# Kernel tuning notes

Measured on AMD Instinct MI355X. Metric: run time of the kernel, lower is better.

The kernel has to match this reference:

```python
import jax, jax.numpy as jnp
import numpy as np
import math

B, CF, H, W = 2, 64, 256, 256
CH = 32          # 'channel' init arg
KS, DIL, PAD = 3, 2, 2
IMG_H, IMG_W = 512, 512


def _pos_encode(h, w, d_model):
    # Sinusoidal encoding along x and y, interleaved sin/cos -> [2*d_model, h, w]
    div = jnp.exp(jnp.arange(0, d_model, 2, dtype=jnp.float32) * (-math.log(10000.0) / d_model))  # [d/2]
    ax = jnp.arange(w, dtype=jnp.float32)[None, :] * div[:, None]   # [d/2, w]
    ay = jnp.arange(h, dtype=jnp.float32)[None, :] * div[:, None]   # [d/2, h]
    x = jnp.stack([jnp.sin(ax), jnp.cos(ax)], axis=1).reshape(d_model, w)  # even=sin, odd=cos
    y = jnp.stack([jnp.sin(ay), jnp.cos(ay)], axis=1).reshape(d_model, h)
    x = jnp.broadcast_to(x[:, None, :], (d_model, h, w))
    y = jnp.broadcast_to(y[:, :, None], (d_model, h, w))
    return jnp.concatenate([x, y], axis=0)  # [2*d_model, h, w]


def _unfold3x3(x):
    # F.unfold(kernel=3, dilation=2, padding=2, stride=1) -> [B, C, 9, H, W]
    b, c, h, w = x.shape
    xp = jnp.pad(x, ((0, 0), (0, 0), (PAD, PAD), (PAD, PAD)))
    offs = (0, DIL, 2 * DIL)
    patches = [xp[:, :, i:i + h, j:j + w] for i in offs for j in offs]  # row-major kernel order
    return jnp.stack(patches, axis=2)


def setup_inputs() -> dict:
    key = jax.random.key(0)
    k1, k2, k3, k4, k5 = jax.random.split(key, 5)
    return {
        "inp": jax.random.normal(k1, (B, CF, H, W), dtype=jnp.float32),
        "img": jax.random.uniform(k2, (B, 3, IMG_H, IMG_W), dtype=jnp.float32),
        "w_pos": jax.random.normal(k3, (CH, 2 * CH), dtype=jnp.float32) * 0.1,
        "w_img": jax.random.normal(k4, (CH, 3), dtype=jnp.float32) * 0.1,
        "w_comp": jax.random.normal(k5, (CF,), dtype=jnp.float32) * 0.1,
    }


def reference(inp, img, w_pos, w_img, w_comp):
    b, cf, h, w = inp.shape
    # positional embedding -> 1x1 conv (channel matmul)
    pos = _pos_encode(h, w, CH)                                   # [2*CH, H, W]
    pos_embd = jnp.einsum('oc,chw->ohw', w_pos, pos)              # [CH, H, W]
    pos_embd = jnp.broadcast_to(pos_embd[None], (b, CH, h, w))
    # bilinear resize of image to feature resolution, then 1x1 conv
    rimg = jax.image.resize(img, (b, 3, h, w), method='bilinear')
    rimg = jnp.einsum('oc,bchw->bohw', w_img, rimg)               # [B, CH, H, W]
    em = jnp.concatenate([rimg, pos_embd], axis=1)                # [B, 2*CH, H, W]
    # neighborhood similarity score
    un_em = _unfold3x3(em)                                        # [B, 2CH, 9, H, W]
    feature_score = jnp.einsum('bckhw,bchw->bkhw', un_em, em)     # [B, 9, H, W]
    # feature compatibility: 1x1 conv (dot with w_comp) per neighbor, sigmoid
    un_fea = _unfold3x3(inp)                                      # [B, CF, 9, H, W]
    comp_score = jax.nn.sigmoid(jnp.einsum('bckhw,c->bkhw', un_fea, w_comp))
    phi = comp_score * feature_score                              # [B, 9, H, W]
    weighted_fea = jnp.einsum('bckhw,bkhw->bchw', un_fea, phi)    # [B, CF, H, W]
    return weighted_fea
```

## Files before the change

kernel.cpp:

```cpp
#include <hip/hip_runtime.h>
#include <math.h>

namespace {
constexpr int Bn = 2, CF = 64;
constexpr int H = 256, W = 256, HW = H * W;
constexpr int IH = 512, IW = 512;

constexpr int OFF_MT   = 0;
constexpr int OFF_GXX  = OFF_MT + 256 * 256;
constexpr int OFF_GYY  = OFF_GXX + 3 * 256;
constexpr int OFF_G    = OFF_GYY + 3 * 256;
constexpr int OFF_RIMG = OFF_G + 16;
constexpr int OFF_S    = OFF_RIMG + Bn * 3 * HW;
constexpr int OFF_PX   = OFF_RIMG;
constexpr int OFF_PY   = OFF_RIMG + 32 * 256;
}

__global__ __launch_bounds__(256) void pxy_kernel(
    const float* __restrict__ w_pos,
    float* __restrict__ PX, float* __restrict__ PY)
{
  const int t = threadIdx.x;
  const int o = blockIdx.x;
  float s[16], c[16];
#pragma unroll
  for (int i = 0; i < 16; i++) {
    float d = expf((float)(2 * i) * (-0.2878231366242557f));
    float a = (float)t * d;
    s[i] = sinf(a);
    c[i] = cosf(a);
  }
  const float* wr = w_pos + o * 64;
  float ax = 0.f, ay = 0.f;
#pragma unroll
  for (int i = 0; i < 16; i++) {
    ax += wr[2 * i] * s[i] + wr[2 * i + 1] * c[i];
    ay += wr[32 + 2 * i] * s[i] + wr[33 + 2 * i] * c[i];
  }
  PX[o * 256 + t] = ax;
  PY[o * 256 + t] = ay;
}

__global__ __launch_bounds__(256) void gram_kernel(
    const float* __restrict__ PX, const float* __restrict__ PY,
    const float* __restrict__ w_img,
    float* __restrict__ Mt, float* __restrict__ GXX, float* __restrict__ GYY,
    float* __restrict__ G)
{
  const int a = threadIdx.x;
  const int t = blockIdx.x;

  float m = 0.f;
#pragma unroll
  for (int o = 0; o < 32; o++) m += PX[o * 256 + a] * PY[o * 256 + t];
  Mt[t * 256 + a] = m;

  if (t == 0) {
#pragma unroll
    for (int j = 0; j < 3; j++) {
      const int nb = a + 2 * (j - 1);
      float gx = 0.f, gy = 0.f;
      if (nb >= 0 && nb < 256) {
#pragma unroll
        for (int o = 0; o < 32; o++) {
          gx += PX[o * 256 + a] * PX[o * 256 + nb];
          gy += PY[o * 256 + a] * PY[o * 256 + nb];
        }
      }
      GXX[j * 256 + a] = gx;
      GYY[j * 256 + a] = gy;
    }
    if (a < 9) {
      const int i = a / 3, j = a % 3;
      float g = 0.f;
#pragma unroll
      for (int o = 0; o < 32; o++) g += w_img[o * 3 + i] * w_img[o * 3 + j];
      G[a] = g;
    }
  }
}

__device__ __forceinline__ void resize_taps(int p, int n, float w[4], int idx[4])
{
#pragma unroll
  for (int r = 0; r < 4; r++) {
    int q = 2 * p - 1 + r;
    idx[r] = min(max(q, 0), 2 * n - 1);
  }
  if (p == 0)          { w[0] = 0.f;        w[1] = 3.f / 7.f; w[2] = 3.f / 7.f; w[3] = 1.f / 7.f; }
  else if (p == n - 1) { w[0] = 1.f / 7.f;  w[1] = 3.f / 7.f; w[2] = 3.f / 7.f; w[3] = 0.f; }
  else                 { w[0] = 0.125f;     w[1] = 0.375f;    w[2] = 0.375f;    w[3] = 0.125f; }
}

__global__ __launch_bounds__(256) void rimg_kernel(
    const float* __restrict__ img, float* __restrict__ rimg)
{
  const int p = blockIdx.x * 256 + threadIdx.x;
  const int c = blockIdx.y;
  const int b = blockIdx.z;
  const int x = p & (W - 1);
  const int y = p >> 8;

  float wy[4], wx[4];
  int ry[4], rx[4];
  resize_taps(y, H, wy, ry);
  resize_taps(x, W, wx, rx);

  const float* ip = img + ((size_t)(b * 3 + c) * IH) * IW;
  float acc = 0.f;
#pragma unroll
  for (int r = 0; r < 4; r++) {
    const float* rowp = ip + ry[r] * IW;
    float rs = wx[0] * rowp[rx[0]] + wx[1] * rowp[rx[1]] +
               wx[2] * rowp[rx[2]] + wx[3] * rowp[rx[3]];
    acc += wy[r] * rs;
  }
  rimg[((size_t)(b * 3 + c)) * HW + p] = acc;
}

__global__ __launch_bounds__(256) void smap_kernel(
    const float* __restrict__ inp, const float* __restrict__ w_comp,
    float* __restrict__ smap)
{
  __shared__ float red[256];
  const int lane = threadIdx.x & 63;
  const int cg = threadIdx.x >> 6;
  const int p = blockIdx.x * 64 + lane;
  const int b = blockIdx.z;

  const float* ib = inp + (size_t)b * CF * HW + (size_t)cg * 16 * HW + p;
  float a0 = 0.f, a1 = 0.f, a2 = 0.f, a3 = 0.f;
#pragma unroll
  for (int c = 0; c < 16; c += 4) {
    a0 += ib[(size_t)(c + 0) * HW] * w_comp[cg * 16 + c + 0];
    a1 += ib[(size_t)(c + 1) * HW] * w_comp[cg * 16 + c + 1];
    a2 += ib[(size_t)(c + 2) * HW] * w_comp[cg * 16 + c + 2];
    a3 += ib[(size_t)(c + 3) * HW] * w_comp[cg * 16 + c + 3];
  }
  red[threadIdx.x] = (a0 + a1) + (a2 + a3);
  __syncthreads();
  if (threadIdx.x < 64) {
    smap[(size_t)b * HW + blockIdx.x * 64 + threadIdx.x] =
        red[threadIdx.x] + red[threadIdx.x + 64] +
        red[threadIdx.x + 128] + red[threadIdx.x + 192];
  }
}

__global__ __launch_bounds__(256) void phigather_kernel(
    const float* __restrict__ inp, const float* __restrict__ rimg,
    const float* __restrict__ smap, const float* __restrict__ Mt,
    const float* __restrict__ GXX, const float* __restrict__ GYY,
    const float* __restrict__ G, float* __restrict__ out)
{
  const int cg = blockIdx.x;
  const int p = blockIdx.y * 256 + threadIdx.x;
  const int b = blockIdx.z;
  const int x = p & (W - 1);
  const int y = p >> 8;

  const float* rb = rimg + (size_t)b * 3 * HW;
  const float r0 = rb[p], r1 = rb[HW + p], r2 = rb[2 * HW + p];
  const float g0 = G[0], g1 = G[1], g2 = G[2];
  const float g3 = G[3], g4 = G[4], g5 = G[5];
  const float g6 = G[6], g7 = G[7], g8 = G[8];
  const float* sb = smap + (size_t)b * HW;

  float ph[9];
  int nb[9];
#pragma unroll
  for (int k = 0; k < 9; k++) {
    const int ky = k / 3, kx = k % 3;
    const int ny = y + 2 * (ky - 1), nx = x + 2 * (kx - 1);
    const bool valid = ((unsigned)ny < (unsigned)H) & ((unsigned)nx < (unsigned)W);
    const int cy = min(max(ny, 0), H - 1);
    const int cx = min(max(nx, 0), W - 1);
    const int np = cy * W + cx;
    nb[k] = np;

    const float n0 = rb[np], n1 = rb[HW + np], n2 = rb[2 * HW + np];
    float fs = r0 * (g0 * n0 + g1 * n1 + g2 * n2)
             + r1 * (g3 * n0 + g4 * n1 + g5 * n2)
             + r2 * (g6 * n0 + g7 * n1 + g8 * n2);
    fs += GXX[kx * 256 + x] + GYY[ky * 256 + y]
        + Mt[y * 256 + cx] + Mt[cy * 256 + x];

    const float s = sb[np];
    const float cs = 1.f / (1.f + expf(-s));
    ph[k] = valid ? cs * fs : 0.f;
  }

  const float* ib = inp + (size_t)b * CF * HW + (size_t)cg * 16 * HW;
  float* ob = out + (size_t)b * CF * HW + (size_t)cg * 16 * HW;
#pragma unroll 4
  for (int c = 0; c < 16; c++) {
    const float* ic = ib + (size_t)c * HW;
    float acc = ph[0] * ic[nb[0]];
#pragma unroll
    for (int k = 1; k < 9; k++) acc += ph[k] * ic[nb[k]];
    ob[(size_t)c * HW + p] = acc;
  }
}

extern "C" void kernel_launch(void* const* d_in, const int* in_sizes, int n_in,
                              void* d_out, int out_size, void* d_ws, size_t ws_size,
                              hipStream_t stream)
{
  const float* inp    = (const float*)d_in[0];
  const float* img    = (const float*)d_in[1];
  const float* w_pos  = (const float*)d_in[2];
  const float* w_img  = (const float*)d_in[3];
  const float* w_comp = (const float*)d_in[4];
  float* out = (float*)d_out;
  float* ws  = (float*)d_ws;

  float* Mt   = ws + OFF_MT;
  float* GXX  = ws + OFF_GXX;
  float* GYY  = ws + OFF_GYY;
  float* G    = ws + OFF_G;
  float* rimg = ws + OFF_RIMG;
  float* smap = ws + OFF_S;
  float* PX   = ws + OFF_PX;
  float* PY   = ws + OFF_PY;

  hipLaunchKernelGGL(pxy_kernel, dim3(32), dim3(256), 0, stream, w_pos, PX, PY);
  hipLaunchKernelGGL(gram_kernel, dim3(256), dim3(256), 0, stream,
                     PX, PY, w_img, Mt, GXX, GYY, G);

  hipLaunchKernelGGL(rimg_kernel, dim3(HW / 256, 3, Bn), dim3(256), 0, stream,
                     img, rimg);
  hipLaunchKernelGGL(smap_kernel, dim3(HW / 64, 1, Bn), dim3(256), 0, stream,
                     inp, w_comp, smap);

  hipLaunchKernelGGL(phigather_kernel, dim3(CF / 16, HW / 256, Bn), dim3(256), 0, stream,
                     inp, rimg, smap, Mt, GXX, GYY, G, out);
}
```

Baseline: 123.2 us.

## Merge resize and score kernels, precompute sigmoid, process two pixels per thread

Combines the image-resize and compatibility-score kernels into one launch, split by block index. The sigmoid is now applied once per pixel when the score map is written, instead of nine times per pixel inside the gather for every channel group. The gather kernel now handles two adjacent pixels per thread with float2 loads and stores, relying on the dilation of 2 keeping both neighbours in the same even-aligned pair. This cuts launch count and redundant transcendental work and widens memory accesses, at the cost of more registers per thread and half as many threads in the gather.

```diff
diff --git a/kernel.cpp b/kernel.cpp
--- a/kernel.cpp
+++ b/kernel.cpp
@@ -92,57 +92,58 @@
   else                 { w[0] = 0.125f;     w[1] = 0.375f;    w[2] = 0.375f;    w[3] = 0.125f; }
 }
 
-__global__ __launch_bounds__(256) void rimg_kernel(
-    const float* __restrict__ img, float* __restrict__ rimg)
-{
-  const int p = blockIdx.x * 256 + threadIdx.x;
-  const int c = blockIdx.y;
+__global__ __launch_bounds__(256) void prep_kernel(
+    const float* __restrict__ img, const float* __restrict__ inp,
+    const float* __restrict__ w_comp,
+    float* __restrict__ rimg, float* __restrict__ smap)
+{
+  const int blk = blockIdx.x;
   const int b = blockIdx.z;
-  const int x = p & (W - 1);
-  const int y = p >> 8;
-
-  float wy[4], wx[4];
-  int ry[4], rx[4];
-  resize_taps(y, H, wy, ry);
-  resize_taps(x, W, wx, rx);
-
-  const float* ip = img + ((size_t)(b * 3 + c) * IH) * IW;
-  float acc = 0.f;
-#pragma unroll
-  for (int r = 0; r < 4; r++) {
-    const float* rowp = ip + ry[r] * IW;
-    float rs = wx[0] * rowp[rx[0]] + wx[1] * rowp[rx[1]] +
-               wx[2] * rowp[rx[2]] + wx[3] * rowp[rx[3]];
-    acc += wy[r] * rs;
-  }
-  rimg[((size_t)(b * 3 + c)) * HW + p] = acc;
-}
-
-__global__ __launch_bounds__(256) void smap_kernel(
-    const float* __restrict__ inp, const float* __restrict__ w_comp,
-    float* __restrict__ smap)
-{
-  __shared__ float red[256];
-  const int lane = threadIdx.x & 63;
-  const int cg = threadIdx.x >> 6;
-  const int p = blockIdx.x * 64 + lane;
-  const int b = blockIdx.z;
-
-  const float* ib = inp + (size_t)b * CF * HW + (size_t)cg * 16 * HW + p;
-  float a0 = 0.f, a1 = 0.f, a2 = 0.f, a3 = 0.f;
-#pragma unroll
-  for (int c = 0; c < 16; c += 4) {
-    a0 += ib[(size_t)(c + 0) * HW] * w_comp[cg * 16 + c + 0];
-    a1 += ib[(size_t)(c + 1) * HW] * w_comp[cg * 16 + c + 1];
-    a2 += ib[(size_t)(c + 2) * HW] * w_comp[cg * 16 + c + 2];
-    a3 += ib[(size_t)(c + 3) * HW] * w_comp[cg * 16 + c + 3];
-  }
-  red[threadIdx.x] = (a0 + a1) + (a2 + a3);
-  __syncthreads();
-  if (threadIdx.x < 64) {
-    smap[(size_t)b * HW + blockIdx.x * 64 + threadIdx.x] =
-        red[threadIdx.x] + red[threadIdx.x + 64] +
-        red[threadIdx.x + 128] + red[threadIdx.x + 192];
+
+  if (blk < 768) {
+    const int c = blk >> 8;
+    const int p = (blk & 255) * 256 + threadIdx.x;
+    const int x = p & (W - 1);
+    const int y = p >> 8;
+
+    float wy[4], wx[4];
+    int ry[4], rx[4];
+    resize_taps(y, H, wy, ry);
+    resize_taps(x, W, wx, rx);
+
+    const float* ip = img + ((size_t)(b * 3 + c) * IH) * IW;
+    float acc = 0.f;
+#pragma unroll
+    for (int r = 0; r < 4; r++) {
+      const float* rowp = ip + ry[r] * IW;
+      float rs = wx[0] * rowp[rx[0]] + wx[1] * rowp[rx[1]] +
+                 wx[2] * rowp[rx[2]] + wx[3] * rowp[rx[3]];
+      acc += wy[r] * rs;
+    }
+    rimg[((size_t)(b * 3 + c)) * HW + p] = acc;
+  } else {
+    __shared__ float red[256];
+    const int sb = blk - 768;
+    const int lane = threadIdx.x & 63;
+    const int cg = threadIdx.x >> 6;
+    const int p = sb * 64 + lane;
+
+    const float* ib = inp + (size_t)b * CF * HW + (size_t)cg * 16 * HW + p;
+    float a0 = 0.f, a1 = 0.f, a2 = 0.f, a3 = 0.f;
+#pragma unroll
+    for (int c = 0; c < 16; c += 4) {
+      a0 += ib[(size_t)(c + 0) * HW] * w_comp[cg * 16 + c + 0];
+      a1 += ib[(size_t)(c + 1) * HW] * w_comp[cg * 16 + c + 1];
+      a2 += ib[(size_t)(c + 2) * HW] * w_comp[cg * 16 + c + 2];
+      a3 += ib[(size_t)(c + 3) * HW] * w_comp[cg * 16 + c + 3];
+    }
+    red[threadIdx.x] = (a0 + a1) + (a2 + a3);
+    __syncthreads();
+    if (threadIdx.x < 64) {
+      const float s = red[threadIdx.x] + red[threadIdx.x + 64] +
+                      red[threadIdx.x + 128] + red[threadIdx.x + 192];
+      smap[(size_t)b * HW + sb * 64 + threadIdx.x] = 1.f / (1.f + expf(-s));
+    }
   }
 }
 
@@ -153,40 +154,54 @@
     const float* __restrict__ G, float* __restrict__ out)
 {
   const int cg = blockIdx.x;
-  const int p = blockIdx.y * 256 + threadIdx.x;
+  const int px = (blockIdx.y * 256 + threadIdx.x) * 2;
   const int b = blockIdx.z;
-  const int x = p & (W - 1);
-  const int y = p >> 8;
+  const int x = px & (W - 1);
+  const int y = px >> 8;
 
   const float* rb = rimg + (size_t)b * 3 * HW;
-  const float r0 = rb[p], r1 = rb[HW + p], r2 = rb[2 * HW + p];
+  const float2 r0 = *(const float2*)(rb + px);
+  const float2 r1 = *(const float2*)(rb + HW + px);
+  const float2 r2 = *(const float2*)(rb + 2 * HW + px);
   const float g0 = G[0], g1 = G[1], g2 = G[2];
   const float g3 = G[3], g4 = G[4], g5 = G[5];
   const float g6 = G[6], g7 = G[7], g8 = G[8];
   const float* sb = smap + (size_t)b * HW;
 
-  float ph[9];
+  float2 ph[9];
   int nb[9];
 #pragma unroll
   for (int k = 0; k < 9; k++) {
     const int ky = k / 3, kx = k % 3;
-    const int ny = y + 2 * (ky - 1), nx = x + 2 * (kx - 1);
+    const int ny = y + 2 * (ky - 1);
+    const int nx = x + 2 * (kx - 1);
     const bool valid = ((unsigned)ny < (unsigned)H) & ((unsigned)nx < (unsigned)W);
     const int cy = min(max(ny, 0), H - 1);
-    const int cx = min(max(nx, 0), W - 1);
-    const int np = cy * W + cx;
+    const int bx = min(max(nx, 0), W - 2);
+    const int np = cy * W + bx;
     nb[k] = np;
 
-    const float n0 = rb[np], n1 = rb[HW + np], n2 = rb[2 * HW + np];
-    float fs = r0 * (g0 * n0 + g1 * n1 + g2 * n2)
-             + r1 * (g3 * n0 + g4 * n1 + g5 * n2)
-             + r2 * (g6 * n0 + g7 * n1 + g8 * n2);
-    fs += GXX[kx * 256 + x] + GYY[ky * 256 + y]
-        + Mt[y * 256 + cx] + Mt[cy * 256 + x];
-
-    const float s = sb[np];
-    const float cs = 1.f / (1.f + expf(-s));
-    ph[k] = valid ? cs * fs : 0.f;
+    const float2 n0 = *(const float2*)(rb + np);
+    const float2 n1 = *(const float2*)(rb + HW + np);
+    const float2 n2 = *(const float2*)(rb + 2 * HW + np);
+    float2 fs;
+    fs.x = r0.x * (g0 * n0.x + g1 * n1.x + g2 * n2.x)
+         + r1.x * (g3 * n0.x + g4 * n1.x + g5 * n2.x)
+         + r2.x * (g6 * n0.x + g7 * n1.x + g8 * n2.x);
+    fs.y = r0.y * (g0 * n0.y + g1 * n1.y + g2 * n2.y)
+         + r1.y * (g3 * n0.y + g4 * n1.y + g5 * n2.y)
+         + r2.y * (g6 * n0.y + g7 * n1.y + g8 * n2.y);
+
+    const float2 gxx = *(const float2*)(GXX + kx * 256 + x);
+    const float gyy = GYY[ky * 256 + y];
+    const float2 mA = *(const float2*)(Mt + y * 256 + bx);
+    const float2 mB = *(const float2*)(Mt + cy * 256 + x);
+    fs.x += gxx.x + gyy + mA.x + mB.x;
+    fs.y += gxx.y + gyy + mA.y + mB.y;
+
+    const float2 sg = *(const float2*)(sb + np);
+    ph[k].x = valid ? sg.x * fs.x : 0.f;
+    ph[k].y = valid ? sg.y * fs.y : 0.f;
   }
 
   const float* ib = inp + (size_t)b * CF * HW + (size_t)cg * 16 * HW;
@@ -194,10 +209,15 @@
 #pragma unroll 4
   for (int c = 0; c < 16; c++) {
     const float* ic = ib + (size_t)c * HW;
-    float acc = ph[0] * ic[nb[0]];
-#pragma unroll
-    for (int k = 1; k < 9; k++) acc += ph[k] * ic[nb[k]];
-    ob[(size_t)c * HW + p] = acc;
+    float2 v = *(const float2*)(ic + nb[0]);
+    float ax = ph[0].x * v.x, ay = ph[0].y * v.y;
+#pragma unroll
+    for (int k = 1; k < 9; k++) {
+      v = *(const float2*)(ic + nb[k]);
+      ax += ph[k].x * v.x;
+      ay += ph[k].y * v.y;
+    }
+    *(float2*)(ob + (size_t)c * HW + px) = make_float2(ax, ay);
   }
 }
 
@@ -226,11 +246,9 @@
   hipLaunchKernelGGL(gram_kernel, dim3(256), dim3(256), 0, stream,
                      PX, PY, w_img, Mt, GXX, GYY, G);
 
-  hipLaunchKernelGGL(rimg_kernel, dim3(HW / 256, 3, Bn), dim3(256), 0, stream,
-                     img, rimg);
-  hipLaunchKernelGGL(smap_kernel, dim3(HW / 64, 1, Bn), dim3(256), 0, stream,
-                     inp, w_comp, smap);
-
-  hipLaunchKernelGGL(phigather_kernel, dim3(CF / 16, HW / 256, Bn), dim3(256), 0, stream,
+  hipLaunchKernelGGL(prep_kernel, dim3(1792, 1, Bn), dim3(256), 0, stream,
+                     img, inp, w_comp, rimg, smap);
+
+  hipLaunchKernelGGL(phigather_kernel, dim3(CF / 16, HW / 512, Bn), dim3(256), 0, stream,
                      inp, rimg, smap, Mt, GXX, GYY, G, out);
 }
```

Measured after the change: 133.4 us. 1.08x slower.
